# Kernel optimization log

Measured on AMD Instinct MI355X. Metric: run time of the kernel, lower is better.

Reference implementation:

```python
import jax, jax.numpy as jnp
import numpy as np

B, NPOS, NNEG, D, NLEM = 8, 512, 512, 128, 32768
MOMENTUM = 0.5
EPS = 1e-12  # F.normalize eps


def setup_inputs() -> dict:
    key = jax.random.key(0)
    k1, k2, k3, k4 = jax.random.split(key, 4)
    x = jax.random.normal(k1, (B, NPOS + NNEG, D), dtype=jnp.float32)
    y = jax.random.randint(k2, (B, NPOS), 0, NPOS).astype(jnp.int64)
    visible = jax.random.randint(k3, (B, NPOS), 0, 2).astype(jnp.int32)
    stdv = 1.0 / np.sqrt(D / 3.0)
    memory = jax.random.uniform(k4, (NLEM, D), dtype=jnp.float32,
                                minval=-stdv, maxval=stdv)
    return {"x": x, "y": y, "visible": visible, "memory": memory, "lru": 3}


def reference(x, y, visible, memory, lru):
    # --- similarity computation (differentiable path) ---
    t = x[:, :NPOS, :]                                  # [B, NPOS, D]
    similarity = jnp.einsum('bpd,md->bpm', t, memory)    # [B, NPOS, NLEM]
    noise_similarity = jnp.einsum('bnd,pd->bnp',
                                  x[:, NPOS:, :], memory[:NPOS])  # [B, NNEG, NPOS]
    y_idx = y.astype(jnp.int64)

    # --- memory bank update (no-grad in original) ---
    vis = visible.astype(x.dtype)[..., None]             # [B, NPOS, 1]
    get = jnp.mean(t * vis, axis=0)                      # [NPOS, D]
    pos_new = memory[:NPOS] * MOMENTUM + get * (1.0 - MOMENTUM)
    neg_flat = x[:, NPOS:, :].reshape(-1, D)             # [B*NNEG, D]
    start = NPOS + lru * NNEG * B                        # lru is a python int
    new_mem = memory.at[start:start + NNEG * B].set(neg_flat)
    new_mem = new_mem.at[:NPOS].set(pos_new)
    norms = jnp.maximum(jnp.linalg.norm(new_mem, axis=1, keepdims=True), EPS)
    new_mem = jax.lax.stop_gradient(new_mem / norms)

    return similarity, y_idx, noise_similarity, new_mem
```

## Files before the change

kernel.cpp:

```cpp
#include <hip/hip_runtime.h>
#include <hip/hip_bf16.h>
#include <cstdint>

#define NPOS 512
#define NNEG 512
#define BATCH 8
#define DDIM 128
#define NLEM 32768
#define NX_ELEM (BATCH * (NPOS + NNEG) * DDIM)
#define NM_ELEM (NLEM * DDIM)

typedef __attribute__((ext_vector_type(4))) float f32x4;
typedef __attribute__((ext_vector_type(16))) float f32x16;
typedef __attribute__((ext_vector_type(8))) short short8;

__device__ __forceinline__ unsigned short f2bf(float f) {
  unsigned u = __float_as_uint(f);
  u = (u + 0x7FFFu + ((u >> 16) & 1u)) >> 16;
  return (unsigned short)u;
}

__device__ __forceinline__ short8 cvt8(f32x4 a0, f32x4 a1) {
  short8 w;
  w[0] = (short)f2bf(a0[0]); w[1] = (short)f2bf(a0[1]);
  w[2] = (short)f2bf(a0[2]); w[3] = (short)f2bf(a0[3]);
  w[4] = (short)f2bf(a1[0]); w[5] = (short)f2bf(a1[1]);
  w[6] = (short)f2bf(a1[2]); w[7] = (short)f2bf(a1[3]);
  return w;
}

__device__ __forceinline__ void async16(const void* g, void* l) {
  __builtin_amdgcn_global_load_lds(
      (const __attribute__((address_space(1))) unsigned int*)g,
      (__attribute__((address_space(3))) unsigned int*)l, 16, 0, 0);
}

__device__ __forceinline__ void newmem_row(int r, int lane, const float* __restrict__ X,
                                           const int* __restrict__ vis,
                                           const float* __restrict__ Mem, int start,
                                           float* __restrict__ out) {
  const int d0 = lane, d1 = lane + 64;
  float v0, v1;
  if (r < NPOS) {
    const float s0 = Mem[(size_t)r * DDIM + d0];
    const float s1 = Mem[(size_t)r * DDIM + d1];
    float a0 = 0.f, a1 = 0.f;
#pragma unroll
    for (int b = 0; b < BATCH; ++b) {
      const float w = (float)vis[b * NPOS + r];
      const float* px = X + (size_t)(b * (NPOS + NNEG) + r) * DDIM;
      a0 += w * px[d0];
      a1 += w * px[d1];
    }
    v0 = 0.5f * s0 + 0.0625f * a0;
    v1 = 0.5f * s1 + 0.0625f * a1;
  } else if (r >= start && r < start + BATCH * NNEG) {
    const int q = r - start;
    const int b = q >> 9, n = q & 511;
    const float* px = X + (size_t)(b * (NPOS + NNEG) + NPOS + n) * DDIM;
    v0 = px[d0];
    v1 = px[d1];
  } else {
    v0 = Mem[(size_t)r * DDIM + d0];
    v1 = Mem[(size_t)r * DDIM + d1];
  }
  float s = v0 * v0 + v1 * v1;
#pragma unroll
  for (int off = 32; off; off >>= 1) s += __shfl_xor(s, off, 64);
  const float inv = 1.0f / fmaxf(sqrtf(s), 1e-12f);
  out[(size_t)r * DDIM + d0] = v0 * inv;
  out[(size_t)r * DDIM + d1] = v1 * inv;
}

__global__ __launch_bounds__(256) void prep_kernel(
    const float* __restrict__ X, const int* __restrict__ y,
    const int* __restrict__ vis, const float* __restrict__ Mem,
    const int* __restrict__ lru_p, unsigned short* __restrict__ xb,
    unsigned short* __restrict__ mb, float* __restrict__ out_y,
    float* __restrict__ out_mem) {
  const int blk = blockIdx.x;
  if (blk < 512) {
    const size_t i = ((size_t)blk * 256 + threadIdx.x) * 8;
    *(short8*)(xb + i) = cvt8(*(const f32x4*)(X + i), *(const f32x4*)(X + i + 4));
  } else if (blk < 2560) {
    const size_t i = ((size_t)(blk - 512) * 256 + threadIdx.x) * 8;
    *(short8*)(mb + i) = cvt8(*(const f32x4*)(Mem + i), *(const f32x4*)(Mem + i + 4));
  } else if (blk < 2576) {
    const int i = (blk - 2560) * 256 + threadIdx.x;
    out_y[i] = (float)y[i];
  } else {
    const int r = (blk - 2576) * 4 + (threadIdx.x >> 6);
    const int start = NPOS + lru_p[0] * (NNEG * BATCH);
    newmem_row(r, threadIdx.x & 63, X, vis, Mem, start, out_mem);
  }
}

__global__ __launch_bounds__(256) void gemm_bf16_kernel(
    const unsigned short* __restrict__ Xb, const unsigned short* __restrict__ Mb,
    float* __restrict__ Csim, float* __restrict__ Cnoise) {
  __shared__ short lds[2 * 128 * 128];
  short* ldsA = lds;
  short* ldsB = lds + 128 * 128;

  const int bx = blockIdx.x, by = blockIdx.y;
  const int m0 = bx * 128;
  int n0, a_off, ldc;
  float* C;
  if (by < 256) { n0 = by * 128; a_off = 0;    C = Csim;   ldc = NLEM; }
  else          { n0 = (by - 256) * 128; a_off = NPOS; C = Cnoise; ldc = NPOS; }
  const int xbase = ((m0 >> 9) << 10) + (m0 & 511) + a_off;

  const int t = threadIdx.x;
  const int lane = t & 63;
  const int wv = t >> 6;

  {
    const int rl = lane >> 4;
    const int slot = lane & 15;
#pragma unroll
    for (int i = 0; i < 8; ++i) {
      const int rowb = wv * 32 + i * 4;
      const int row = rowb + rl;
      const int ss = slot ^ (row & 15);
      async16(Xb + (size_t)(xbase + row) * DDIM + ss * 8, &ldsA[rowb * 128]);
      async16(Mb + (size_t)(n0 + row) * DDIM + ss * 8, &ldsB[rowb * 128]);
    }
  }
  __syncthreads();

  const int wr = wv >> 1, wc = wv & 1;
  const int la = lane & 31, lb = lane >> 5;

  f32x16 acc[2][2] = {};
#pragma unroll
  for (int kk = 0; kk < 8; ++kk) {
    short8 af[2], bfr[2];
#pragma unroll
    for (int m2 = 0; m2 < 2; ++m2) {
      const int row = wr * 64 + m2 * 32 + la;
      const int ss = ((kk * 2 + lb) ^ (row & 15)) * 8;
      af[m2] = *(const short8*)&ldsA[row * 128 + ss];
    }
#pragma unroll
    for (int n2 = 0; n2 < 2; ++n2) {
      const int row = wc * 64 + n2 * 32 + la;
      const int ss = ((kk * 2 + lb) ^ (row & 15)) * 8;
      bfr[n2] = *(const short8*)&ldsB[row * 128 + ss];
    }
#pragma unroll
    for (int m2 = 0; m2 < 2; ++m2)
#pragma unroll
      for (int n2 = 0; n2 < 2; ++n2)
        acc[m2][n2] = __builtin_amdgcn_mfma_f32_32x32x16_bf16(
            af[m2], bfr[n2], acc[m2][n2], 0, 0, 0);
  }

#pragma unroll
  for (int m2 = 0; m2 < 2; ++m2) {
#pragma unroll
    for (int n2 = 0; n2 < 2; ++n2) {
      const int col = n0 + wc * 64 + n2 * 32 + la;
      const int rbase = m0 + wr * 64 + m2 * 32 + lb * 4;
#pragma unroll
      for (int r = 0; r < 16; ++r) {
        const int row = rbase + (r & 3) + 8 * (r >> 2);
        C[(size_t)row * ldc + col] = acc[m2][n2][r];
      }
    }
  }
}

__global__ __launch_bounds__(256) void gemm_conv_kernel(
    const float* __restrict__ X, const float* __restrict__ Bm,
    float* __restrict__ C, int ldc, int a_off) {
  __shared__ short lds[2 * 128 * 128];
  short* ldsA = lds;
  short* ldsB = lds + 128 * 128;
  const int t = threadIdx.x;
  const int m0 = blockIdx.x * 128;
  const int n0 = blockIdx.y * 128;
  const int slot = t & 15;
  const int rsub = t >> 4;
#pragma unroll
  for (int it = 0; it < 8; ++it) {
    const int row = it * 16 + rsub;
    const int gr = m0 + row;
    const int xrow = ((gr >> 9) << 10) + (gr & 511) + a_off;
    const f32x4* pa = (const f32x4*)(X + (size_t)xrow * DDIM + slot * 8);
    const f32x4* pb = (const f32x4*)(Bm + (size_t)(n0 + row) * DDIM + slot * 8);
    short8 wa = cvt8(pa[0], pa[1]);
    short8 wb = cvt8(pb[0], pb[1]);
    const int ss = (slot ^ (row & 15)) * 8;
    *(short8*)&ldsA[row * 128 + ss] = wa;
    *(short8*)&ldsB[row * 128 + ss] = wb;
  }
  __syncthreads();
  const int lane = t & 63;
  const int wv = t >> 6;
  const int wr = wv >> 1, wc = wv & 1;
  const int la = lane & 31, lb = lane >> 5;
  f32x16 acc[2][2] = {};
#pragma unroll
  for (int kk = 0; kk < 8; ++kk) {
    short8 af[2], bfr[2];
#pragma unroll
    for (int m2 = 0; m2 < 2; ++m2) {
      const int row = wr * 64 + m2 * 32 + la;
      const int ss = ((kk * 2 + lb) ^ (row & 15)) * 8;
      af[m2] = *(const short8*)&ldsA[row * 128 + ss];
    }
#pragma unroll
    for (int n2 = 0; n2 < 2; ++n2) {
      const int row = wc * 64 + n2 * 32 + la;
      const int ss = ((kk * 2 + lb) ^ (row & 15)) * 8;
      bfr[n2] = *(const short8*)&ldsB[row * 128 + ss];
    }
#pragma unroll
    for (int m2 = 0; m2 < 2; ++m2)
#pragma unroll
      for (int n2 = 0; n2 < 2; ++n2)
        acc[m2][n2] = __builtin_amdgcn_mfma_f32_32x32x16_bf16(
            af[m2], bfr[n2], acc[m2][n2], 0, 0, 0);
  }
#pragma unroll
  for (int m2 = 0; m2 < 2; ++m2)
#pragma unroll
    for (int n2 = 0; n2 < 2; ++n2) {
      const int col = n0 + wc * 64 + n2 * 32 + la;
      const int rbase = m0 + wr * 64 + m2 * 32 + lb * 4;
#pragma unroll
      for (int r = 0; r < 16; ++r) {
        const int row = rbase + (r & 3) + 8 * (r >> 2);
        C[(size_t)row * ldc + col] = acc[m2][n2][r];
      }
    }
}

__global__ void y_kernel(const int* __restrict__ y, float* __restrict__ out) {
  const int i = blockIdx.x * blockDim.x + threadIdx.x;
  if (i < BATCH * NPOS) out[i] = (float)y[i];
}

__global__ __launch_bounds__(256) void newmem_kernel(
    const float* __restrict__ X, const int* __restrict__ vis,
    const float* __restrict__ Mem, const int* __restrict__ lru_p,
    float* __restrict__ out) {
  const int r = blockIdx.x * 4 + (threadIdx.x >> 6);
  const int start = NPOS + lru_p[0] * (NNEG * BATCH);
  newmem_row(r, threadIdx.x & 63, X, vis, Mem, start, out);
}

extern "C" void kernel_launch(void* const* d_in, const int* in_sizes, int n_in,
                              void* d_out, int out_size, void* d_ws, size_t ws_size,
                              hipStream_t stream) {
  const float* x = (const float*)d_in[0];
  const int* y = (const int*)d_in[1];
  const int* visible = (const int*)d_in[2];
  const float* memory = (const float*)d_in[3];
  const int* lru = (const int*)d_in[4];
  float* out = (float*)d_out;

  const size_t OFF_Y = (size_t)BATCH * NPOS * NLEM;
  const size_t OFF_NOISE = OFF_Y + (size_t)BATCH * NPOS;
  const size_t OFF_MEM = OFF_NOISE + (size_t)BATCH * NNEG * NPOS;

  const size_t need = (size_t)(NX_ELEM + NM_ELEM) * 2;
  if (ws_size >= need) {
    unsigned short* xb = (unsigned short*)d_ws;
    unsigned short* mb = xb + NX_ELEM;
    prep_kernel<<<2576 + NLEM / 4, 256, 0, stream>>>(
        x, y, visible, memory, lru, xb, mb, out + OFF_Y, out + OFF_MEM);
    gemm_bf16_kernel<<<dim3(32, 260), 256, 0, stream>>>(
        xb, mb, out, out + OFF_NOISE);
  } else {
    gemm_conv_kernel<<<dim3(32, 256), 256, 0, stream>>>(x, memory, out, NLEM, 0);
    gemm_conv_kernel<<<dim3(32, 4), 256, 0, stream>>>(x, memory, out + OFF_NOISE, NPOS, NPOS);
    y_kernel<<<16, 256, 0, stream>>>(y, out + OFF_Y);
    newmem_kernel<<<NLEM / 4, 256, 0, stream>>>(x, visible, memory, lru, out + OFF_MEM);
  }
}
```

Baseline: 130.4 us.

## Convert bf16 GEMM to persistent kernel with double-buffered LDS prefetch

Replaces the 32x260 one-tile-per-block GEMM grid with a persistent grid of 256 blocks. Each block walks the 8320 output tiles in a strided loop. While the current tile's MFMAs and output stores run, the next tile's A/B operands are prefetched asynchronously into a second LDS buffer, with partial vmcnt waits and barriers between iterations. The goal is to hide global load latency and cut block launch overhead. The cost is that the doubled LDS (128KB per block) limits occupancy to one block per CU, which may hurt issue of the very large store stream that dominates this kernel.

```diff
diff --git a/kernel.cpp b/kernel.cpp
--- a/kernel.cpp
+++ b/kernel.cpp
@@ -9,6 +9,8 @@
 #define NLEM 32768
 #define NX_ELEM (BATCH * (NPOS + NNEG) * DDIM)
 #define NM_ELEM (NLEM * DDIM)
+#define GRID_GEMM 256
+#define NT_TILES 8320
 
 typedef __attribute__((ext_vector_type(4))) float f32x4;
 typedef __attribute__((ext_vector_type(16))) float f32x16;
@@ -95,78 +97,100 @@
   }
 }
 
-__global__ __launch_bounds__(256) void gemm_bf16_kernel(
+__global__ __launch_bounds__(256) void gemm_persist_kernel(
     const unsigned short* __restrict__ Xb, const unsigned short* __restrict__ Mb,
     float* __restrict__ Csim, float* __restrict__ Cnoise) {
-  __shared__ short lds[2 * 128 * 128];
-  short* ldsA = lds;
-  short* ldsB = lds + 128 * 128;
-
-  const int bx = blockIdx.x, by = blockIdx.y;
-  const int m0 = bx * 128;
-  int n0, a_off, ldc;
-  float* C;
-  if (by < 256) { n0 = by * 128; a_off = 0;    C = Csim;   ldc = NLEM; }
-  else          { n0 = (by - 256) * 128; a_off = NPOS; C = Cnoise; ldc = NPOS; }
-  const int xbase = ((m0 >> 9) << 10) + (m0 & 511) + a_off;
+  __shared__ short lds[2][2][128 * 128];
 
   const int t = threadIdx.x;
-  const int lane = t & 63;
-  const int wv = t >> 6;
-
-  {
-    const int rl = lane >> 4;
-    const int slot = lane & 15;
+  const int lane = t & 63, wv = t >> 6;
+  const int rl = lane >> 4, slot = lane & 15;
+  const int wr = wv >> 1, wc = wv & 1;
+  const int la = lane & 31, lb = lane >> 5;
+
+  const int b = blockIdx.x;
+  const int nk = (NT_TILES - b + GRID_GEMM - 1) / GRID_GEMM;
+
+  auto stage = [&](int p, int T) {
+    const int m0 = (T & 31) * 128;
+    const int by = T >> 5;
+    const int n0 = (by < 256 ? by : by - 256) * 128;
+    const int a_off = (by < 256) ? 0 : NPOS;
+    const int xbase = ((m0 >> 9) << 10) + (m0 & 511) + a_off;
+    short* A = lds[p][0];
+    short* B = lds[p][1];
 #pragma unroll
     for (int i = 0; i < 8; ++i) {
       const int rowb = wv * 32 + i * 4;
       const int row = rowb + rl;
       const int ss = slot ^ (row & 15);
-      async16(Xb + (size_t)(xbase + row) * DDIM + ss * 8, &ldsA[rowb * 128]);
-      async16(Mb + (size_t)(n0 + row) * DDIM + ss * 8, &ldsB[rowb * 128]);
-    }
-  }
-  __syncthreads();
-
-  const int wr = wv >> 1, wc = wv & 1;
-  const int la = lane & 31, lb = lane >> 5;
-
-  f32x16 acc[2][2] = {};
-#pragma unroll
-  for (int kk = 0; kk < 8; ++kk) {
-    short8 af[2], bfr[2];
+      async16(Xb + (size_t)(xbase + row) * DDIM + ss * 8, &A[rowb * 128]);
+      async16(Mb + (size_t)(n0 + row) * DDIM + ss * 8, &B[rowb * 128]);
+    }
+  };
+
+  stage(0, b);
+  asm volatile("s_waitcnt vmcnt(0)" ::: "memory");
+  __builtin_amdgcn_s_barrier();
+  __builtin_amdgcn_sched_barrier(0);
+
+  int p = 0;
+  for (int k = 0; k < nk; ++k) {
+    const int T = b + k * GRID_GEMM;
+    if (k + 1 < nk) stage(p ^ 1, T + GRID_GEMM);
+
+    const short* A = lds[p][0];
+    const short* B = lds[p][1];
+    f32x16 acc[2][2] = {};
+#pragma unroll
+    for (int kk = 0; kk < 8; ++kk) {
+      short8 af[2], bfr[2];
+#pragma unroll
+      for (int m2 = 0; m2 < 2; ++m2) {
+        const int row = wr * 64 + m2 * 32 + la;
+        const int ss = ((kk * 2 + lb) ^ (row & 15)) * 8;
+        af[m2] = *(const short8*)&A[row * 128 + ss];
+      }
+#pragma unroll
+      for (int n2 = 0; n2 < 2; ++n2) {
+        const int row = wc * 64 + n2 * 32 + la;
+        const int ss = ((kk * 2 + lb) ^ (row & 15)) * 8;
+        bfr[n2] = *(const short8*)&B[row * 128 + ss];
+      }
+#pragma unroll
+      for (int m2 = 0; m2 < 2; ++m2)
+#pragma unroll
+        for (int n2 = 0; n2 < 2; ++n2)
+          acc[m2][n2] = __builtin_amdgcn_mfma_f32_32x32x16_bf16(
+              af[m2], bfr[n2], acc[m2][n2], 0, 0, 0);
+    }
+
+    const int m0 = (T & 31) * 128;
+    const int by = T >> 5;
+    float* C;
+    int ldc, n0c;
+    if (by < 256) { C = Csim; ldc = NLEM; n0c = by * 128; }
+    else          { C = Cnoise; ldc = NPOS; n0c = (by - 256) * 128; }
 #pragma unroll
     for (int m2 = 0; m2 < 2; ++m2) {
-      const int row = wr * 64 + m2 * 32 + la;
-      const int ss = ((kk * 2 + lb) ^ (row & 15)) * 8;
-      af[m2] = *(const short8*)&ldsA[row * 128 + ss];
-    }
-#pragma unroll
-    for (int n2 = 0; n2 < 2; ++n2) {
-      const int row = wc * 64 + n2 * 32 + la;
-      const int ss = ((kk * 2 + lb) ^ (row & 15)) * 8;
-      bfr[n2] = *(const short8*)&ldsB[row * 128 + ss];
-    }
-#pragma unroll
-    for (int m2 = 0; m2 < 2; ++m2)
-#pragma unroll
-      for (int n2 = 0; n2 < 2; ++n2)
-        acc[m2][n2] = __builtin_amdgcn_mfma_f32_32x32x16_bf16(
-            af[m2], bfr[n2], acc[m2][n2], 0, 0, 0);
-  }
-
-#pragma unroll
-  for (int m2 = 0; m2 < 2; ++m2) {
-#pragma unroll
-    for (int n2 = 0; n2 < 2; ++n2) {
-      const int col = n0 + wc * 64 + n2 * 32 + la;
-      const int rbase = m0 + wr * 64 + m2 * 32 + lb * 4;
-#pragma unroll
-      for (int r = 0; r < 16; ++r) {
-        const int row = rbase + (r & 3) + 8 * (r >> 2);
-        C[(size_t)row * ldc + col] = acc[m2][n2][r];
+#pragma unroll
+      for (int n2 = 0; n2 < 2; ++n2) {
+        const int col = n0c + wc * 64 + n2 * 32 + la;
+        const int rbase = m0 + wr * 64 + m2 * 32 + lb * 4;
+#pragma unroll
+        for (int r = 0; r < 16; ++r) {
+          const int row = rbase + (r & 3) + 8 * (r >> 2);
+          C[(size_t)row * ldc + col] = acc[m2][n2][r];
+        }
       }
     }
+
+    if (k + 1 < nk) {
+      asm volatile("s_waitcnt vmcnt(60)" ::: "memory");
+      __builtin_amdgcn_s_barrier();
+      __builtin_amdgcn_sched_barrier(0);
+    }
+    p ^= 1;
   }
 }
 
@@ -270,7 +294,7 @@
     unsigned short* mb = xb + NX_ELEM;
     prep_kernel<<<2576 + NLEM / 4, 256, 0, stream>>>(
         x, y, visible, memory, lru, xb, mb, out + OFF_Y, out + OFF_MEM);
-    gemm_bf16_kernel<<<dim3(32, 260), 256, 0, stream>>>(
+    gemm_persist_kernel<<<GRID_GEMM, 256, 0, stream>>>(
         xb, mb, out, out + OFF_NOISE);
   } else {
     gemm_conv_kernel<<<dim3(32, 256), 256, 0, stream>>>(x, memory, out, NLEM, 0);
```

Measured after the change: 132.1 us. Within noise of the previous version (+1.3%).
